# Performance work log

Hardware: AMD Instinct MI355X
Metric: run time of the kernel (lower is better)

## Reference

```python
import jax, jax.numpy as jnp
import numpy as np

N_NODES = 18870
HIDDEN = 256
K = 20
HEAD_HIDDEN = 512
N_CLASSES = 3
N_GENES_OUT = 6640
B = 1024
FALLBACK_SCALE = 1e-3
LN_EPS = 1e-5


def setup_inputs() -> dict:
    key = jax.random.key(0)
    ks = jax.random.split(key, 8)
    node_idx = jax.random.randint(ks[0], (B,), 0, N_NODES)
    topk_neighbors = jax.random.randint(ks[1], (N_NODES, K), 0, N_NODES)
    node_emb = jax.random.normal(ks[2], (N_NODES, HIDDEN), dtype=jnp.float32)
    fallback_emb = jax.random.normal(ks[3], (HIDDEN,), dtype=jnp.float32) * 0.02
    w_attn = jax.random.normal(ks[4], (HIDDEN,), dtype=jnp.float32) * 0.02
    ln_gamma = jnp.ones((2 * HIDDEN,), dtype=jnp.float32)
    ln_beta = jnp.zeros((2 * HIDDEN,), dtype=jnp.float32)
    W1 = jax.random.normal(ks[5], (2 * HIDDEN, HEAD_HIDDEN), dtype=jnp.float32) * 0.02
    b1 = jnp.zeros((HEAD_HIDDEN,), dtype=jnp.float32)
    W2 = jax.random.normal(ks[6], (HEAD_HIDDEN, N_CLASSES * N_GENES_OUT), dtype=jnp.float32) * 0.02
    b2 = jnp.zeros((N_CLASSES * N_GENES_OUT,), dtype=jnp.float32)
    return dict(node_idx=node_idx, topk_neighbors=topk_neighbors, node_emb=node_emb,
                fallback_emb=fallback_emb, w_attn=w_attn, ln_gamma=ln_gamma, ln_beta=ln_beta,
                W1=W1, b1=b1, W2=W2, b2=b2)


def reference(node_idx, topk_neighbors, node_emb, fallback_emb, w_attn,
              ln_gamma, ln_beta, W1, b1, W2, b2):
    valid = node_idx >= 0                                   # [B]
    safe_idx = jnp.where(valid, node_idx, 0)                # [B]
    graph_emb = node_emb[safe_idx]                          # [B, H]
    pert_emb = jnp.where(valid[:, None],
                         graph_emb + FALLBACK_SCALE * fallback_emb[None, :],
                         fallback_emb[None, :])              # [B, H]

    nbr_idx = topk_neighbors[safe_idx]                      # [B, K]
    valid_nbr = nbr_idx >= 0                                # [B, K]
    nbr_emb = node_emb[jnp.clip(nbr_idx, 0)]                # [B, K, H]
    nbr_emb = nbr_emb * valid_nbr[..., None].astype(nbr_emb.dtype)

    # Faithful to the original broadcast: scores[b,k] = pert_emb[b,0] * (nbr_emb[b,k] . w_attn)
    scores = pert_emb[:, 0:1] * jnp.einsum('bkh,h->bk', nbr_emb, w_attn)  # [B, K]
    scores = jnp.where(valid_nbr, scores, -1e9)
    has_valid = jnp.any(valid_nbr, axis=1, keepdims=True)   # [B, 1]
    attn = jnp.where(has_valid, jax.nn.softmax(scores, axis=-1),
                     jnp.zeros_like(scores))                # [B, K]
    context = jnp.einsum('bk,bkh->bh', attn, nbr_emb)       # [B, H]

    combined = jnp.concatenate([pert_emb, context], axis=-1)  # [B, 2H]
    mu = jnp.mean(combined, axis=-1, keepdims=True)
    var = jnp.mean(jnp.square(combined - mu), axis=-1, keepdims=True)
    x = (combined - mu) * jax.lax.rsqrt(var + LN_EPS) * ln_gamma + ln_beta
    h = jax.nn.gelu(x @ W1 + b1, approximate=False)          # [B, HH]
    logits = h @ W2 + b2                                     # [B, 3*6640]
    return logits.reshape(-1, N_CLASSES, N_GENES_OUT)


if __name__ == '__main__':
    out = reference(**setup_inputs())
    print(out.shape)
```

## Files before the change

### kernel.cpp

```cpp
#include <hip/hip_runtime.h>
#include <hip/hip_bf16.h>
#include <math.h>

#define HIDDEN 256
#define K_NBR 20
#define NB 1024

typedef __bf16 bf16x8 __attribute__((ext_vector_type(8)));
typedef float f32x4 __attribute__((ext_vector_type(4)));

__device__ __forceinline__ float wave_sum(float v) {
#pragma unroll
    for (int o = 32; o > 0; o >>= 1) v += __shfl_xor(v, o, 64);
    return v;
}

__device__ __forceinline__ void gload16(const void* g, void* l) {
    __builtin_amdgcn_global_load_lds(
        (const __attribute__((address_space(1))) void*)g,
        (__attribute__((address_space(3))) void*)l, 16, 0, 0);
}

__device__ __forceinline__ int swz3(int g, int row) {
    return (g & ~7) | ((g & 7) ^ (row & 7));
}

__device__ __forceinline__ void attn_ln_body(
    int b, int t, const int* __restrict__ node_idx, const int* __restrict__ topk,
    const float* __restrict__ node_emb, const float* __restrict__ fallback,
    const float* __restrict__ w_attn, const float* __restrict__ gamma,
    const float* __restrict__ beta, __bf16* __restrict__ xb,
    float* pe, float (*nbr)[HIDDEN], int* nidx, float* sc, float* red)
{
    int lane = t & 63, w = t >> 6;
    int nid = node_idx[b];
    bool valid = nid >= 0;
    int safe = valid ? nid : 0;

    pe[t] = valid ? node_emb[(size_t)safe * HIDDEN + t] + 1e-3f * fallback[t]
                  : fallback[t];
    if (t < K_NBR) nidx[t] = topk[safe * K_NBR + t];
    __syncthreads();
    for (int r = 0; r < K_NBR; ++r) {
        int gi = nidx[r];
        nbr[r][t] = (gi >= 0) ? node_emb[(size_t)gi * HIDDEN + t] : 0.f;
    }
    __syncthreads();
    float pe0 = pe[0];
    float wa[4];
#pragma unroll
    for (int q = 0; q < 4; ++q) wa[q] = w_attn[lane + 64 * q];
    for (int k = w; k < K_NBR; k += 4) {
        float p = 0.f;
#pragma unroll
        for (int q = 0; q < 4; ++q) p += nbr[k][lane + 64 * q] * wa[q];
        p = wave_sum(p);
        if (lane == 0) sc[k] = (nidx[k] >= 0) ? pe0 * p : -1e9f;
    }
    __syncthreads();
    bool has_valid = false;
#pragma unroll
    for (int k = 0; k < K_NBR; ++k) has_valid |= (nidx[k] >= 0);
    float mx = -1e30f;
#pragma unroll
    for (int k = 0; k < K_NBR; ++k) mx = fmaxf(mx, sc[k]);
    float at[K_NBR];
    float s = 0.f;
#pragma unroll
    for (int k = 0; k < K_NBR; ++k) { at[k] = expf(sc[k] - mx); s += at[k]; }
    float inv = has_valid ? 1.f / s : 0.f;
    float ctx = 0.f;
#pragma unroll
    for (int k = 0; k < K_NBR; ++k) ctx += (at[k] * inv) * nbr[k][t];
    float v0 = pe[t], v1 = ctx;
    float s1 = wave_sum(v0 + v1);
    float s2 = wave_sum(v0 * v0 + v1 * v1);
    if (lane == 0) { red[w] = s1; red[4 + w] = s2; }
    __syncthreads();
    s1 = red[0] + red[1] + red[2] + red[3];
    s2 = red[4] + red[5] + red[6] + red[7];
    float mu = s1 / 512.f;
    float var = s2 / 512.f - mu * mu;
    float rs = rsqrtf(var + 1e-5f);
    size_t base = (size_t)b * 512;
    int mask = b & 7;
    {
        int e = t;
        int g = e >> 3, off = e & 7;
        int gp = (g & ~7) | ((g & 7) ^ mask);
        xb[base + gp * 8 + off] = (__bf16)((v0 - mu) * rs * gamma[t] + beta[t]);
        e = 256 + t;
        g = e >> 3;
        gp = (g & ~7) | ((g & 7) ^ mask);
        xb[base + gp * 8 + off] = (__bf16)((v1 - mu) * rs * gamma[256 + t] + beta[256 + t]);
    }
}

__device__ __forceinline__ void transpose_body(
    const float* __restrict__ Wm, __bf16* __restrict__ WT,
    int Kd, int Nd, int Np, int bx, int by, int t)
{
    int n = bx * 64 + (t >> 2);
    int k0 = by * 32 + (t & 3) * 8;
    bool ok = n < Nd;
    bf16x8 v;
#pragma unroll
    for (int j = 0; j < 8; ++j) {
        float f = ok ? Wm[(size_t)(k0 + j) * Nd + n] : 0.f;
        v[j] = (__bf16)f;
    }
    if (n < Np) {
        int gp = swz3(k0 >> 3, n);
        *(bf16x8*)(WT + (size_t)n * Kd + gp * 8) = v;
    }
}

__global__ __launch_bounds__(256) void prep_kernel(
    const int* __restrict__ node_idx, const int* __restrict__ topk,
    const float* __restrict__ node_emb, const float* __restrict__ fallback,
    const float* __restrict__ w_attn, const float* __restrict__ gamma,
    const float* __restrict__ beta, const float* __restrict__ W1,
    const float* __restrict__ W2, __bf16* __restrict__ xb,
    __bf16* __restrict__ w1t, __bf16* __restrict__ w2t)
{
    __shared__ float pe[HIDDEN];
    __shared__ float nbr[K_NBR][HIDDEN];
    __shared__ int   nidx[K_NBR];
    __shared__ float sc[K_NBR];
    __shared__ float red[8];
    int bid = blockIdx.x;
    int t = threadIdx.x;
    if (bid < 1024) {
        attn_ln_body(bid, t, node_idx, topk, node_emb, fallback, w_attn, gamma,
                     beta, xb, pe, nbr, nidx, sc, red);
        return;
    }
    bid -= 1024;
    if (bid < 128) { transpose_body(W1, w1t, 512, 512, 512, bid % 8, bid / 8, t); return; }
    bid -= 128;
    transpose_body(W2, w2t, 512, 19920, 19968, bid % 312, bid / 312, t);
}

__global__ __launch_bounds__(256, 4) void gemm1_kernel(
    const __bf16* __restrict__ A, const __bf16* __restrict__ BT,
    const float* __restrict__ bias, __bf16* __restrict__ Cb,
    int M, int N, int K)
{
    constexpr int BK = 64;
    __shared__ __bf16 As[2][64 * BK];
    __shared__ __bf16 Bs[2][64 * BK];

    int t = threadIdx.x;
    int lane = t & 63;
    int wid = t >> 6;
    int wm = wid >> 1, wn = wid & 1;
    int lo = lane & 15, hi = lane >> 4;

    int nwg = gridDim.x;
    int bid = blockIdx.x;
    int cpx = nwg >> 3;
    int lid = (bid & 7) * cpx + (bid >> 3);
    int m0 = (lid & 15) * 64;
    int n0 = (lid >> 4) * 64;

    int rsub = lane >> 3, kc = lane & 7;

    auto STAGE = [&](int buf, int k0) {
#pragma unroll
        for (int j = 0; j < 2; ++j) {
            int rb = j * 32 + wid * 8;
            gload16(A + (size_t)(m0 + rb + rsub) * K + k0 + kc * 8, &As[buf][rb * BK]);
        }
#pragma unroll
        for (int j = 0; j < 2; ++j) {
            int rb = j * 32 + wid * 8;
            gload16(BT + (size_t)(n0 + rb + rsub) * K + k0 + kc * 8, &Bs[buf][rb * BK]);
        }
    };

    f32x4 acc[2][2];
#pragma unroll
    for (int m = 0; m < 2; ++m)
#pragma unroll
        for (int n = 0; n < 2; ++n) acc[m][n] = (f32x4){0.f, 0.f, 0.f, 0.f};

    auto COMPUTE = [&](int buf) {
#pragma unroll
        for (int ks = 0; ks < 2; ++ks) {
            bf16x8 af[2], bfr[2];
#pragma unroll
            for (int m = 0; m < 2; ++m) {
                int r = wm * 32 + m * 16 + lo;
                af[m] = *(const bf16x8*)&As[buf][r * BK + (((ks * 4 + hi) ^ (r & 7)) * 8)];
            }
#pragma unroll
            for (int n = 0; n < 2; ++n) {
                int r = wn * 32 + n * 16 + lo;
                bfr[n] = *(const bf16x8*)&Bs[buf][r * BK + (((ks * 4 + hi) ^ (r & 7)) * 8)];
            }
#pragma unroll
            for (int m = 0; m < 2; ++m)
#pragma unroll
                for (int n = 0; n < 2; ++n)
                    acc[m][n] = __builtin_amdgcn_mfma_f32_16x16x32_bf16(
                        af[m], bfr[n], acc[m][n], 0, 0, 0);
        }
    };

    const int nt = K / BK;
    STAGE(0, 0);
    for (int tt = 0; tt < nt - 1; ++tt) {
        STAGE((tt + 1) & 1, (tt + 1) * BK);
        asm volatile("s_waitcnt vmcnt(4)" ::: "memory");
        __builtin_amdgcn_s_barrier();
        __builtin_amdgcn_sched_barrier(0);
        COMPUTE(tt & 1);
        __builtin_amdgcn_sched_barrier(0);
        __builtin_amdgcn_s_barrier();
    }
    asm volatile("s_waitcnt vmcnt(0)" ::: "memory");
    __builtin_amdgcn_s_barrier();
    __builtin_amdgcn_sched_barrier(0);
    COMPUTE((nt - 1) & 1);

#pragma unroll
    for (int m = 0; m < 2; ++m) {
        int gr = m0 + wm * 32 + m * 16 + hi * 4;
#pragma unroll
        for (int n = 0; n < 2; ++n) {
            int gc = n0 + wn * 32 + n * 16 + lo;
            float bv = bias[gc];
#pragma unroll
            for (int r = 0; r < 4; ++r) {
                float v = acc[m][n][r] + bv;
                float g = v * 0.5f * (1.f + erff(v * 0.70710678118f));
                int row = gr + r;
                int gp = swz3(gc >> 3, row);
                Cb[(size_t)row * N + gp * 8 + (gc & 7)] = (__bf16)g;
            }
        }
    }
}

__global__ __launch_bounds__(512, 6) void gemm2_kernel(
    const __bf16* __restrict__ A, const __bf16* __restrict__ BT,
    const float* __restrict__ bias, float* __restrict__ C,
    int M, int N, int K)
{
    constexpr int BK = 64;
    __shared__ __bf16 As[2][64 * BK];
    __shared__ __bf16 Bs[2][128 * BK];

    int t = threadIdx.x;
    int lane = t & 63;
    int wid = t >> 6;
    int wm = wid >> 2, wn = wid & 3;
    int lo = lane & 15, hi = lane >> 4;

    int nwg = gridDim.x;
    int bid = blockIdx.x;
    int cpx = nwg >> 3;
    int lid = (bid & 7) * cpx + (bid >> 3);
    int m0 = (lid & 15) * 64;
    int n0 = (lid >> 4) * 128;

    int rsub = lane >> 3, kc = lane & 7;

    auto STAGE = [&](int buf, int k0) {
        gload16(A + (size_t)(m0 + wid * 8 + rsub) * K + k0 + kc * 8,
                &As[buf][(wid * 8) * BK]);
#pragma unroll
        for (int j = 0; j < 2; ++j) {
            int rb = j * 64 + wid * 8;
            gload16(BT + (size_t)(n0 + rb + rsub) * K + k0 + kc * 8, &Bs[buf][rb * BK]);
        }
    };

    f32x4 acc[2][2];
#pragma unroll
    for (int m = 0; m < 2; ++m)
#pragma unroll
        for (int n = 0; n < 2; ++n) acc[m][n] = (f32x4){0.f, 0.f, 0.f, 0.f};

    auto COMPUTE = [&](int buf) {
#pragma unroll
        for (int ks = 0; ks < 2; ++ks) {
            bf16x8 af[2], bfr[2];
#pragma unroll
            for (int m = 0; m < 2; ++m) {
                int r = wm * 32 + m * 16 + lo;
                af[m] = *(const bf16x8*)&As[buf][r * BK + (((ks * 4 + hi) ^ (r & 7)) * 8)];
            }
#pragma unroll
            for (int n = 0; n < 2; ++n) {
                int r = wn * 32 + n * 16 + lo;
                bfr[n] = *(const bf16x8*)&Bs[buf][r * BK + (((ks * 4 + hi) ^ (r & 7)) * 8)];
            }
#pragma unroll
            for (int m = 0; m < 2; ++m)
#pragma unroll
                for (int n = 0; n < 2; ++n)
                    acc[m][n] = __builtin_amdgcn_mfma_f32_16x16x32_bf16(
                        af[m], bfr[n], acc[m][n], 0, 0, 0);
        }
    };

    const int nt = K / BK;
    STAGE(0, 0);
    for (int tt = 0; tt < nt - 1; ++tt) {
        STAGE((tt + 1) & 1, (tt + 1) * BK);
        asm volatile("s_waitcnt vmcnt(3)" ::: "memory");
        __builtin_amdgcn_s_barrier();
        __builtin_amdgcn_sched_barrier(0);
        COMPUTE(tt & 1);
        __builtin_amdgcn_sched_barrier(0);
        __builtin_amdgcn_s_barrier();
    }
    asm volatile("s_waitcnt vmcnt(0)" ::: "memory");
    __builtin_amdgcn_s_barrier();
    __builtin_amdgcn_sched_barrier(0);
    COMPUTE((nt - 1) & 1);

#pragma unroll
    for (int m = 0; m < 2; ++m) {
        int gr = m0 + wm * 32 + m * 16 + hi * 4;
#pragma unroll
        for (int n = 0; n < 2; ++n) {
            int gc = n0 + wn * 32 + n * 16 + lo;
            if (gc < N) {
                float bv = bias[gc];
#pragma unroll
                for (int r = 0; r < 4; ++r)
                    C[(size_t)(gr + r) * N + gc] = acc[m][n][r] + bv;
            }
        }
    }
}

extern "C" void kernel_launch(void* const* d_in, const int* in_sizes, int n_in,
                              void* d_out, int out_size, void* d_ws, size_t ws_size,
                              hipStream_t stream) {
    const int*   node_idx = (const int*)d_in[0];
    const int*   topk     = (const int*)d_in[1];
    const float* node_emb = (const float*)d_in[2];
    const float* fallback = (const float*)d_in[3];
    const float* w_attn   = (const float*)d_in[4];
    const float* gamma    = (const float*)d_in[5];
    const float* beta     = (const float*)d_in[6];
    const float* W1       = (const float*)d_in[7];
    const float* b1       = (const float*)d_in[8];
    const float* W2       = (const float*)d_in[9];
    const float* b2       = (const float*)d_in[10];
    float* out = (float*)d_out;

    const int M = 1024, Kd = 512, N1 = 512, N2 = 19920;

    __bf16* xb  = (__bf16*)d_ws;
    __bf16* h   = xb + (size_t)M * Kd;
    __bf16* w1t = h + (size_t)M * Kd;
    __bf16* w2t = w1t + (size_t)N1 * Kd;

    prep_kernel<<<1024 + 128 + 4992, 256, 0, stream>>>(
        node_idx, topk, node_emb, fallback, w_attn, gamma, beta, W1, W2,
        xb, w1t, w2t);

    gemm1_kernel<<<dim3(128), 256, 0, stream>>>(
        xb, w1t, b1, h, M, N1, Kd);

    gemm2_kernel<<<dim3(2496), 512, 0, stream>>>(
        h, w2t, b2, out, M, N2, Kd);
    (void)ws_size;
}
```

Baseline: 69.23 us.

## Overlap the first GEMM with the W2 transpose by regrouping kernel launches

The launch schedule is reorganized. The first kernel now does only the attention/LayerNorm and the W1 transpose, and a second kernel runs the GELU GEMM1 blocks alongside the large W2 bf16 transpose blocks. The standalone gemm1 launch is removed, so the small 128-block GEMM1 no longer runs alone on a mostly idle GPU. In exchange, the W2 transpose now starts only after the attention kernel finishes, and the GEMM1 blocks lose their tile-remapping swizzle.

```diff
diff --git a/kernel.cpp b/kernel.cpp
--- a/kernel.cpp
+++ b/kernel.cpp
@@ -115,13 +115,109 @@
     }
 }
 
-__global__ __launch_bounds__(256) void prep_kernel(
+template<bool GELU>
+__device__ __forceinline__ void gemm64_body(
+    int m0, int n0, int t,
+    const __bf16* __restrict__ A, const __bf16* __restrict__ BT,
+    const float* __restrict__ bias, __bf16* __restrict__ Cb, float* __restrict__ Cf,
+    int N, int K, __bf16 (*As)[64 * 64], __bf16 (*Bs)[64 * 64])
+{
+    constexpr int BK = 64;
+    int lane = t & 63;
+    int wid = t >> 6;
+    int wm = wid >> 1, wn = wid & 1;
+    int lo = lane & 15, hi = lane >> 4;
+    int rsub = lane >> 3, kc = lane & 7;
+
+    auto STAGE = [&](int buf, int k0) {
+#pragma unroll
+        for (int j = 0; j < 2; ++j) {
+            int rb = j * 32 + wid * 8;
+            gload16(A + (size_t)(m0 + rb + rsub) * K + k0 + kc * 8, &As[buf][rb * BK]);
+        }
+#pragma unroll
+        for (int j = 0; j < 2; ++j) {
+            int rb = j * 32 + wid * 8;
+            gload16(BT + (size_t)(n0 + rb + rsub) * K + k0 + kc * 8, &Bs[buf][rb * BK]);
+        }
+    };
+
+    f32x4 acc[2][2];
+#pragma unroll
+    for (int m = 0; m < 2; ++m)
+#pragma unroll
+        for (int n = 0; n < 2; ++n) acc[m][n] = (f32x4){0.f, 0.f, 0.f, 0.f};
+
+    auto COMPUTE = [&](int buf) {
+#pragma unroll
+        for (int ks = 0; ks < 2; ++ks) {
+            bf16x8 af[2], bfr[2];
+#pragma unroll
+            for (int m = 0; m < 2; ++m) {
+                int r = wm * 32 + m * 16 + lo;
+                af[m] = *(const bf16x8*)&As[buf][r * BK + (((ks * 4 + hi) ^ (r & 7)) * 8)];
+            }
+#pragma unroll
+            for (int n = 0; n < 2; ++n) {
+                int r = wn * 32 + n * 16 + lo;
+                bfr[n] = *(const bf16x8*)&Bs[buf][r * BK + (((ks * 4 + hi) ^ (r & 7)) * 8)];
+            }
+#pragma unroll
+            for (int m = 0; m < 2; ++m)
+#pragma unroll
+                for (int n = 0; n < 2; ++n)
+                    acc[m][n] = __builtin_amdgcn_mfma_f32_16x16x32_bf16(
+                        af[m], bfr[n], acc[m][n], 0, 0, 0);
+        }
+    };
+
+    const int nt = K / BK;
+    STAGE(0, 0);
+    for (int tt = 0; tt < nt - 1; ++tt) {
+        STAGE((tt + 1) & 1, (tt + 1) * BK);
+        asm volatile("s_waitcnt vmcnt(4)" ::: "memory");
+        __builtin_amdgcn_s_barrier();
+        __builtin_amdgcn_sched_barrier(0);
+        COMPUTE(tt & 1);
+        __builtin_amdgcn_sched_barrier(0);
+        __builtin_amdgcn_s_barrier();
+    }
+    asm volatile("s_waitcnt vmcnt(0)" ::: "memory");
+    __builtin_amdgcn_s_barrier();
+    __builtin_amdgcn_sched_barrier(0);
+    COMPUTE((nt - 1) & 1);
+
+#pragma unroll
+    for (int m = 0; m < 2; ++m) {
+        int gr = m0 + wm * 32 + m * 16 + hi * 4;
+#pragma unroll
+        for (int n = 0; n < 2; ++n) {
+            int gc = n0 + wn * 32 + n * 16 + lo;
+            if (gc < N) {
+                float bv = bias[gc];
+#pragma unroll
+                for (int r = 0; r < 4; ++r) {
+                    float v = acc[m][n][r] + bv;
+                    if constexpr (GELU) {
+                        float g = v * 0.5f * (1.f + erff(v * 0.70710678118f));
+                        int row = gr + r;
+                        int gp = swz3(gc >> 3, row);
+                        Cb[(size_t)row * N + gp * 8 + (gc & 7)] = (__bf16)g;
+                    } else {
+                        Cf[(size_t)(gr + r) * N + gc] = v;
+                    }
+                }
+            }
+        }
+    }
+}
+
+__global__ __launch_bounds__(256) void prep1_kernel(
     const int* __restrict__ node_idx, const int* __restrict__ topk,
     const float* __restrict__ node_emb, const float* __restrict__ fallback,
     const float* __restrict__ w_attn, const float* __restrict__ gamma,
     const float* __restrict__ beta, const float* __restrict__ W1,
-    const float* __restrict__ W2, __bf16* __restrict__ xb,
-    __bf16* __restrict__ w1t, __bf16* __restrict__ w2t)
+    __bf16* __restrict__ xb, __bf16* __restrict__ w1t)
 {
     __shared__ float pe[HIDDEN];
     __shared__ float nbr[K_NBR][HIDDEN];
@@ -136,110 +232,26 @@
         return;
     }
     bid -= 1024;
-    if (bid < 128) { transpose_body(W1, w1t, 512, 512, 512, bid % 8, bid / 8, t); return; }
+    transpose_body(W1, w1t, 512, 512, 512, bid % 8, bid / 8, t);
+}
+
+__global__ __launch_bounds__(256) void prep2_kernel(
+    const float* __restrict__ W2, __bf16* __restrict__ w2t,
+    const __bf16* __restrict__ xb, const __bf16* __restrict__ w1t,
+    const float* __restrict__ b1, __bf16* __restrict__ h)
+{
+    __shared__ __bf16 As[2][64 * 64];
+    __shared__ __bf16 Bs[2][64 * 64];
+    int bid = blockIdx.x;
+    int t = threadIdx.x;
+    if (bid < 128) {
+        int m0 = (bid & 15) * 64;
+        int n0 = (bid >> 4) * 64;
+        gemm64_body<true>(m0, n0, t, xb, w1t, b1, h, nullptr, 512, 512, As, Bs);
+        return;
+    }
     bid -= 128;
     transpose_body(W2, w2t, 512, 19920, 19968, bid % 312, bid / 312, t);
-}
-
-__global__ __launch_bounds__(256, 4) void gemm1_kernel(
-    const __bf16* __restrict__ A, const __bf16* __restrict__ BT,
-    const float* __restrict__ bias, __bf16* __restrict__ Cb,
-    int M, int N, int K)
-{
-    constexpr int BK = 64;
-    __shared__ __bf16 As[2][64 * BK];
-    __shared__ __bf16 Bs[2][64 * BK];
-
-    int t = threadIdx.x;
-    int lane = t & 63;
-    int wid = t >> 6;
-    int wm = wid >> 1, wn = wid & 1;
-    int lo = lane & 15, hi = lane >> 4;
-
-    int nwg = gridDim.x;
-    int bid = blockIdx.x;
-    int cpx = nwg >> 3;
-    int lid = (bid & 7) * cpx + (bid >> 3);
-    int m0 = (lid & 15) * 64;
-    int n0 = (lid >> 4) * 64;
-
-    int rsub = lane >> 3, kc = lane & 7;
-
-    auto STAGE = [&](int buf, int k0) {
-#pragma unroll
-        for (int j = 0; j < 2; ++j) {
-            int rb = j * 32 + wid * 8;
-            gload16(A + (size_t)(m0 + rb + rsub) * K + k0 + kc * 8, &As[buf][rb * BK]);
-        }
-#pragma unroll
-        for (int j = 0; j < 2; ++j) {
-            int rb = j * 32 + wid * 8;
-            gload16(BT + (size_t)(n0 + rb + rsub) * K + k0 + kc * 8, &Bs[buf][rb * BK]);
-        }
-    };
-
-    f32x4 acc[2][2];
-#pragma unroll
-    for (int m = 0; m < 2; ++m)
-#pragma unroll
-        for (int n = 0; n < 2; ++n) acc[m][n] = (f32x4){0.f, 0.f, 0.f, 0.f};
-
-    auto COMPUTE = [&](int buf) {
-#pragma unroll
-        for (int ks = 0; ks < 2; ++ks) {
-            bf16x8 af[2], bfr[2];
-#pragma unroll
-            for (int m = 0; m < 2; ++m) {
-                int r = wm * 32 + m * 16 + lo;
-                af[m] = *(const bf16x8*)&As[buf][r * BK + (((ks * 4 + hi) ^ (r & 7)) * 8)];
-            }
-#pragma unroll
-            for (int n = 0; n < 2; ++n) {
-                int r = wn * 32 + n * 16 + lo;
-                bfr[n] = *(const bf16x8*)&Bs[buf][r * BK + (((ks * 4 + hi) ^ (r & 7)) * 8)];
-            }
-#pragma unroll
-            for (int m = 0; m < 2; ++m)
-#pragma unroll
-                for (int n = 0; n < 2; ++n)
-                    acc[m][n] = __builtin_amdgcn_mfma_f32_16x16x32_bf16(
-                        af[m], bfr[n], acc[m][n], 0, 0, 0);
-        }
-    };
-
-    const int nt = K / BK;
-    STAGE(0, 0);
-    for (int tt = 0; tt < nt - 1; ++tt) {
-        STAGE((tt + 1) & 1, (tt + 1) * BK);
-        asm volatile("s_waitcnt vmcnt(4)" ::: "memory");
-        __builtin_amdgcn_s_barrier();
-        __builtin_amdgcn_sched_barrier(0);
-        COMPUTE(tt & 1);
-        __builtin_amdgcn_sched_barrier(0);
-        __builtin_amdgcn_s_barrier();
-    }
-    asm volatile("s_waitcnt vmcnt(0)" ::: "memory");
-    __builtin_amdgcn_s_barrier();
-    __builtin_amdgcn_sched_barrier(0);
-    COMPUTE((nt - 1) & 1);
-
-#pragma unroll
-    for (int m = 0; m < 2; ++m) {
-        int gr = m0 + wm * 32 + m * 16 + hi * 4;
-#pragma unroll
-        for (int n = 0; n < 2; ++n) {
-            int gc = n0 + wn * 32 + n * 16 + lo;
-            float bv = bias[gc];
-#pragma unroll
-            for (int r = 0; r < 4; ++r) {
-                float v = acc[m][n][r] + bv;
-                float g = v * 0.5f * (1.f + erff(v * 0.70710678118f));
-                int row = gr + r;
-                int gp = swz3(gc >> 3, row);
-                Cb[(size_t)row * N + gp * 8 + (gc & 7)] = (__bf16)g;
-            }
-        }
-    }
 }
 
 __global__ __launch_bounds__(512, 6) void gemm2_kernel(
@@ -360,12 +372,11 @@
     __bf16* w1t = h + (size_t)M * Kd;
     __bf16* w2t = w1t + (size_t)N1 * Kd;
 
-    prep_kernel<<<1024 + 128 + 4992, 256, 0, stream>>>(
-        node_idx, topk, node_emb, fallback, w_attn, gamma, beta, W1, W2,
-        xb, w1t, w2t);
-
-    gemm1_kernel<<<dim3(128), 256, 0, stream>>>(
-        xb, w1t, b1, h, M, N1, Kd);
+    prep1_kernel<<<1024 + 128, 256, 0, stream>>>(
+        node_idx, topk, node_emb, fallback, w_attn, gamma, beta, W1, xb, w1t);
+
+    prep2_kernel<<<128 + 4992, 256, 0, stream>>>(
+        W2, w2t, xb, w1t, b1, h);
 
     gemm2_kernel<<<dim3(2496), 512, 0, stream>>>(
         h, w2t, b2, out, M, N2, Kd);
```

Result: slower. 74.33 us (+7.4%).
